# Optimization experiments

Measured on AMD Instinct MI355X. Metric: run time of the kernel, lower is better.

The kernel has to match this reference:

```python
import jax, jax.numpy as jnp
import numpy as np

DIM = 192
RES = 64
NUM_HEADS = 4
H_SP, W_SP = RES, 4  # idx == 0
SCALE = (DIM // NUM_HEADS) ** (-0.5)


def conv2d(x, w, b, pad, groups=1):
    y = jax.lax.conv_general_dilated(
        x, w, window_strides=(1, 1), padding=[(pad, pad), (pad, pad)],
        dimension_numbers=("NCHW", "OIHW", "NCHW"), feature_group_count=groups)
    return y + b[None, :, None, None]


def img2windows(img, H_sp, W_sp):
    B, C, H, W = img.shape
    x = img.reshape(B, C, H // H_sp, H_sp, W // W_sp, W_sp)
    return jnp.transpose(x, (0, 2, 4, 3, 5, 1)).reshape(-1, H_sp * W_sp, C)


def windows2img(w, H_sp, W_sp, H, W):
    Bw = w.shape[0]
    B = Bw // ((H // H_sp) * (W // W_sp))
    x = w.reshape(B, H // H_sp, W // W_sp, H_sp, W_sp, -1)
    return jnp.transpose(x, (0, 5, 1, 3, 2, 4)).reshape(B, -1, H, W)


def im2cswin(x):
    w = img2windows(x, H_SP, W_SP)  # [B', L, C]
    Bw, L, C = w.shape
    return jnp.transpose(w.reshape(Bw, L, NUM_HEADS, C // NUM_HEADS), (0, 2, 1, 3))


def setup_inputs() -> dict:
    key = jax.random.key(0)
    ks = jax.random.split(key, 11)
    s = 0.02
    return {
        "x": jax.random.normal(ks[0], (32, DIM, RES, RES), jnp.float32),
        "w_qk": jax.random.normal(ks[1], (2 * DIM, DIM, 1, 1), jnp.float32) * s,
        "b_qk": jnp.zeros((2 * DIM,), jnp.float32),
        "w_q5": jax.random.normal(ks[2], (DIM, 1, 5, 5), jnp.float32) * s,
        "b_q5": jnp.zeros((DIM,), jnp.float32),
        "w_k5": jax.random.normal(ks[3], (DIM, 1, 5, 5), jnp.float32) * s,
        "b_k5": jnp.zeros((DIM,), jnp.float32),
        "w_v": jax.random.normal(ks[4], (DIM, DIM, 1, 1), jnp.float32) * s,
        "b_v": jnp.zeros((DIM,), jnp.float32),
        "w_cape": jax.random.normal(ks[5], (DIM, 1, 5, 5), jnp.float32) * s,
        "b_cape": jnp.zeros((DIM,), jnp.float32),
    }


def reference(x, w_qk, b_qk, w_q5, b_q5, w_k5, b_k5, w_v, b_v, w_cape, b_cape):
    B, C, H, W = x.shape
    qk = conv2d(x, w_qk, b_qk, pad=0)
    q, k = jnp.split(qk, 2, axis=1)
    v = conv2d(x, w_v, b_v, pad=0)
    cape = conv2d(v, w_cape, b_cape, pad=2, groups=DIM)  # depthwise 5x5
    q = im2cswin(conv2d(q, w_q5, b_q5, pad=2, groups=DIM) + cape)
    k = im2cswin(conv2d(k, w_k5, b_k5, pad=2, groups=DIM) + cape)
    vw = im2cswin(v)
    q = q * SCALE
    attn = jnp.einsum("whqd,whkd->whqk", q, k)  # windows, heads, L, L
    attn = jax.nn.softmax(attn, axis=-1)
    out = jnp.einsum("whqk,whkd->whqd", attn, vw)
    Bw = out.shape[0]
    out = jnp.transpose(out, (0, 2, 1, 3)).reshape(Bw, H_SP * W_SP, C)
    return windows2img(out, H_SP, W_SP, H, W) + cape
```

## Files before the change

kernel.cpp:

```cpp
#include <hip/hip_runtime.h>

typedef short short8 __attribute__((ext_vector_type(8)));
typedef float f32x4 __attribute__((ext_vector_type(4)));
typedef int i32x4 __attribute__((ext_vector_type(4)));
typedef uint4 uint4_a4 __attribute__((aligned(4)));
typedef uint2 uint2_a4 __attribute__((aligned(4)));

#define BATCH 32
#define DIM 192
#define RES 64
#define HW 4096
#define NH 4
#define DH 48
#define NWIN 16
#define LTOK 256
#define BUFE (BATCH * DIM * HW)
#define SCALE_Q 0.14433756729740643f
#define LOG2E 1.4426950408889634f

__device__ __forceinline__ unsigned short f2bf(float f) {
  unsigned int u = __builtin_bit_cast(unsigned int, f);
  u += 0x7fffu + ((u >> 16) & 1u);
  return (unsigned short)(u >> 16);
}
__device__ __forceinline__ float bf2f(unsigned short h) {
  unsigned int u = ((unsigned int)h) << 16;
  return __builtin_bit_cast(float, u);
}
__device__ __forceinline__ f32x4 mfma16(short8 a, short8 b, f32x4 c) {
  return __builtin_amdgcn_mfma_f32_16x16x32_bf16(a, b, c, 0, 0, 0);
}

__global__ __launch_bounds__(256) void k0_wcvt(
    const float* __restrict__ w_qk, const float* __restrict__ w_v,
    unsigned short* __restrict__ wbf) {
  int u = blockIdx.x * 256 + threadIdx.x;
  int i4 = u * 4;
  const float* src = (i4 < 2 * DIM * DIM) ? (w_qk + i4) : (w_v + (i4 - 2 * DIM * DIM));
  float4 f = *(const float4*)src;
  uint2 pk;
  pk.x = (unsigned int)f2bf(f.x) | ((unsigned int)f2bf(f.y) << 16);
  pk.y = (unsigned int)f2bf(f.z) | ((unsigned int)f2bf(f.w) << 16);
  *(uint2*)&wbf[i4] = pk;
}

__global__ __launch_bounds__(256, 2) void k1_conv1x1(
    const float* __restrict__ x, const unsigned short* __restrict__ wbf,
    const float* __restrict__ b_qk, const float* __restrict__ b_v,
    unsigned short* __restrict__ q_raw, unsigned short* __restrict__ k_raw,
    unsigned short* __restrict__ v_buf) {
  __shared__ unsigned short Al[96 * 200];
  __shared__ unsigned short Bl[64 * 200];
  __shared__ unsigned short Os[96 * 68];
  const int tid = threadIdx.x;
  const int pix0 = blockIdx.x * 64;
  const int b = blockIdx.y;

  {
    const float* xb = x + (size_t)b * (DIM * HW) + pix0;
    int px = tid & 63;
    int icq = tid >> 6;
    for (int it = 0; it < 6; ++it) {
      int ic8 = icq + it * 4;
      const float* p = xb + (size_t)(ic8 * 8) * HW + px;
      unsigned short h[8];
#pragma unroll
      for (int j = 0; j < 8; ++j) h[j] = f2bf(p[(size_t)j * HW]);
      uint4 pk;
      pk.x = h[0] | ((unsigned int)h[1] << 16);
      pk.y = h[2] | ((unsigned int)h[3] << 16);
      pk.z = h[4] | ((unsigned int)h[5] << 16);
      pk.w = h[6] | ((unsigned int)h[7] << 16);
      *(uint4*)&Bl[px * 200 + ic8 * 8] = pk;
    }
  }

  const int lane = tid & 63, wv = tid >> 6;
  const int quad = lane >> 4, col = lane & 15;
  const int m0 = (wv >> 1) * 48, n0 = (wv & 1) * 32;

  for (int t = 0; t < 6; ++t) {
    {
      const unsigned short* wsrc = wbf + t * (96 * 192);
      uint4 tmp[9];
#pragma unroll
      for (int it = 0; it < 9; ++it) {
        int row = (it * 256 + tid) / 24, part = (it * 256 + tid) % 24;
        tmp[it] = *(const uint4*)(wsrc + row * 192 + part * 8);
      }
#pragma unroll
      for (int it = 0; it < 9; ++it) {
        int row = (it * 256 + tid) / 24, part = (it * 256 + tid) % 24;
        *(uint4*)&Al[row * 200 + part * 8] = tmp[it];
      }
    }
    __syncthreads();

    f32x4 acc[3][2];
#pragma unroll
    for (int fm = 0; fm < 3; ++fm)
#pragma unroll
      for (int fn = 0; fn < 2; ++fn) {
        acc[fm][fn][0] = 0.f; acc[fm][fn][1] = 0.f;
        acc[fm][fn][2] = 0.f; acc[fm][fn][3] = 0.f;
      }

#pragma unroll
    for (int ks = 0; ks < 6; ++ks) {
      short8 a[3], bb[2];
#pragma unroll
      for (int fm = 0; fm < 3; ++fm)
        a[fm] = *(const short8*)&Al[(m0 + fm * 16 + col) * 200 + ks * 32 + quad * 8];
#pragma unroll
      for (int fn = 0; fn < 2; ++fn)
        bb[fn] = *(const short8*)&Bl[(n0 + fn * 16 + col) * 200 + ks * 32 + quad * 8];
#pragma unroll
      for (int fm = 0; fm < 3; ++fm)
#pragma unroll
        for (int fn = 0; fn < 2; ++fn) acc[fm][fn] = mfma16(a[fm], bb[fn], acc[fm][fn]);
    }

    const int oc0 = t * 96;
#pragma unroll
    for (int fm = 0; fm < 3; ++fm) {
#pragma unroll
      for (int r = 0; r < 4; ++r) {
        int ocoff = m0 + fm * 16 + quad * 4 + r;
        int ocg = oc0 + ocoff;
        float bias = (ocg < 384) ? b_qk[ocg] : b_v[ocg - 384];
#pragma unroll
        for (int fn = 0; fn < 2; ++fn) {
          int px = n0 + fn * 16 + col;
          Os[ocoff * 68 + px] = f2bf(acc[fm][fn][r] + bias);
        }
      }
    }
    __syncthreads();

    unsigned short* dst;
    int ocbase;
    if (oc0 < 192) { dst = q_raw; ocbase = oc0; }
    else if (oc0 < 384) { dst = k_raw; ocbase = oc0 - 192; }
    else { dst = v_buf; ocbase = oc0 - 384; }
    {
      int row0 = tid >> 3, part = tid & 7;
#pragma unroll
      for (int it = 0; it < 3; ++it) {
        int row = it * 32 + row0;
        *(uint4*)&dst[((size_t)b * DIM + (ocbase + row)) * HW + pix0 + part * 8] =
            *(const uint4*)&Os[row * 68 + part * 8];
      }
    }
  }
}

__global__ __launch_bounds__(256) void k2_cape(
    const unsigned short* __restrict__ v_buf, const float* __restrict__ w_cape,
    const float* __restrict__ b_cape, float* __restrict__ cape_out) {
  const int c = blockIdx.y, b = blockIdx.z;
  const int h = blockIdx.x * 16 + (threadIdx.x >> 4);
  const int w4 = threadIdx.x & 15;
  const unsigned short* vp = v_buf + ((size_t)b * DIM + c) * HW;
  float wk[25];
#pragma unroll
  for (int i = 0; i < 25; ++i) wk[i] = w_cape[c * 25 + i];
  float acc[4];
  float bz = b_cape[c];
  acc[0] = acc[1] = acc[2] = acc[3] = bz;
#pragma unroll
  for (int dy = 0; dy < 5; ++dy) {
    int hr = h + dy - 2;
    float row[8];
    if (hr >= 0 && hr < RES) {
      const unsigned short* rp = vp + hr * RES + w4 * 4 - 2;
      uint4 pk;
      pk.x = pk.y = pk.z = pk.w = 0u;
      if (w4 == 0) {
        uint2_a4 m = *(const uint2_a4*)(rp + 2);
        pk.y = m.x; pk.z = m.y;
        pk.w = *(const unsigned int*)(rp + 6);
      } else if (w4 == 15) {
        pk.x = *(const unsigned int*)rp;
        uint2_a4 m = *(const uint2_a4*)(rp + 2);
        pk.y = m.x; pk.z = m.y;
      } else {
        pk = *(const uint4_a4*)rp;
      }
      row[0] = bf2f((unsigned short)(pk.x & 0xffff));
      row[1] = bf2f((unsigned short)(pk.x >> 16));
      row[2] = bf2f((unsigned short)(pk.y & 0xffff));
      row[3] = bf2f((unsigned short)(pk.y >> 16));
      row[4] = bf2f((unsigned short)(pk.z & 0xffff));
      row[5] = bf2f((unsigned short)(pk.z >> 16));
      row[6] = bf2f((unsigned short)(pk.w & 0xffff));
      row[7] = bf2f((unsigned short)(pk.w >> 16));
    } else {
#pragma unroll
      for (int j = 0; j < 8; ++j) row[j] = 0.f;
    }
#pragma unroll
    for (int wj = 0; wj < 4; ++wj)
#pragma unroll
      for (int dx = 0; dx < 5; ++dx) acc[wj] += row[wj + dx] * wk[dy * 5 + dx];
  }
  float4 o;
  o.x = acc[0]; o.y = acc[1]; o.z = acc[2]; o.w = acc[3];
  *(float4*)&cape_out[((size_t)b * DIM + c) * HW + h * RES + w4 * 4] = o;
}

__global__ __launch_bounds__(256) void k3_dw(
    const unsigned short* __restrict__ src, const float* __restrict__ w5,
    const float* __restrict__ b5, const float* __restrict__ cape,
    unsigned short* __restrict__ dst_w, float scale) {
  __shared__ unsigned short patch[64 * 168];
  __shared__ unsigned short outS[64 * 72];
  const int lid = blockIdx.x;
  const int xx = lid & 7;
  const int ii = lid >> 3;
  const int b = xx * 4 + ii / 192;
  const int rem = ii % 192;
  const int wb = rem / 12;
  const int rr2 = rem % 12;
  const int ct = rr2 >> 2, ht = rr2 & 3;
  const int c0 = ct * 64, h0 = ht * 16;
  const int tid = threadIdx.x;

  const int c = tid >> 2, hq = tid & 3;
  float wk[25];
#pragma unroll
  for (int i = 0; i < 25; ++i) wk[i] = w5[(c0 + c) * 25 + i];
  float bz = b5[c0 + c];
  const size_t cpbase = ((size_t)b * DIM + c0 + c) * HW + (size_t)wb * 4;
  float4 cp4[4];
#pragma unroll
  for (int j = 0; j < 4; ++j)
    cp4[j] = *(const float4*)&cape[cpbase + (size_t)(h0 + hq * 4 + j) * RES];

  for (int it = 0; it < 5; ++it) {
    int u = it * 256 + tid;
    int cc = u / 20, rr = u % 20;
    int hr = h0 - 2 + rr;
    uint4 pk;
    pk.x = pk.y = pk.z = pk.w = 0u;
    if (hr >= 0 && hr < RES) {
      const unsigned short* rp =
          src + ((size_t)b * DIM + c0 + cc) * HW + hr * RES + wb * 4 - 2;
      if (wb == 0) {
        uint2_a4 m = *(const uint2_a4*)(rp + 2);
        pk.y = m.x; pk.z = m.y;
        pk.w = *(const unsigned int*)(rp + 6);
      } else if (wb == 15) {
        pk.x = *(const unsigned int*)rp;
        uint2_a4 m = *(const uint2_a4*)(rp + 2);
        pk.y = m.x; pk.z = m.y;
      } else {
        pk = *(const uint4_a4*)rp;
      }
    }
    *(uint4*)&patch[cc * 168 + rr * 8] = pk;
  }
  __syncthreads();

  float acc[4][4];
#pragma unroll
  for (int j = 0; j < 4; ++j)
#pragma unroll
    for (int wm = 0; wm < 4; ++wm) acc[j][wm] = bz;

#pragma unroll
  for (int rel = 0; rel < 8; ++rel) {
    int p = hq * 4 + rel;
    uint4 pk = *(const uint4*)&patch[c * 168 + p * 8];
    float f8[8];
    f8[0] = bf2f((unsigned short)(pk.x & 0xffff));
    f8[1] = bf2f((unsigned short)(pk.x >> 16));
    f8[2] = bf2f((unsigned short)(pk.y & 0xffff));
    f8[3] = bf2f((unsigned short)(pk.y >> 16));
    f8[4] = bf2f((unsigned short)(pk.z & 0xffff));
    f8[5] = bf2f((unsigned short)(pk.z >> 16));
    f8[6] = bf2f((unsigned short)(pk.w & 0xffff));
    f8[7] = bf2f((unsigned short)(pk.w >> 16));
#pragma unroll
    for (int j = 0; j < 4; ++j) {
      int dy = rel - j;
      if (dy >= 0 && dy <= 4) {
#pragma unroll
        for (int wm = 0; wm < 4; ++wm)
#pragma unroll
          for (int dx = 0; dx < 5; ++dx) acc[j][wm] += f8[wm + dx] * wk[dy * 5 + dx];
      }
    }
  }

#pragma unroll
  for (int j = 0; j < 4; ++j) {
    float4 cp = cp4[j];
    int lb = (hq * 4 + j) * 4;
    outS[(lb + 0) * 72 + c] = f2bf((acc[j][0] + cp.x) * scale);
    outS[(lb + 1) * 72 + c] = f2bf((acc[j][1] + cp.y) * scale);
    outS[(lb + 2) * 72 + c] = f2bf((acc[j][2] + cp.z) * scale);
    outS[(lb + 3) * 72 + c] = f2bf((acc[j][3] + cp.w) * scale);
  }
  __syncthreads();

  const size_t obase = ((size_t)(b * NWIN + wb) * LTOK + (size_t)h0 * 4) * DIM + c0;
  for (int it = 0; it < 2; ++it) {
    int u = it * 256 + tid;
    int ll = u >> 3, part = u & 7;
    *(uint4*)&dst_w[obase + (size_t)ll * DIM + part * 8] =
        *(const uint4*)&outS[ll * 72 + part * 8];
  }
}

#define KSTR 56
#define VSTR 256

__global__ __launch_bounds__(256, 3) void k5_attn(
    const unsigned short* __restrict__ qf_w, const unsigned short* __restrict__ kf_w,
    const unsigned short* __restrict__ v_buf, unsigned short* __restrict__ out_w) {
  __shared__ unsigned short smem[26624];
  unsigned short* Kl = smem;
  unsigned short* Vl = smem + 14336;

  const int lid = blockIdx.x;
  const int xx = lid & 7;
  const int ii = lid >> 3;
  const int b = (xx << 2) | (ii >> 6);
  const int rem = ii & 63;
  const int wb = rem >> 2;
  const int hd = rem & 3;
  const int wi = b * NWIN + wb;

  const int tid = threadIdx.x, lane = tid & 63, wv = tid >> 6;
  const int quad = lane >> 4, col = lane & 15;

  short8 z8 = {0, 0, 0, 0, 0, 0, 0, 0};
  const unsigned short* qbase =
      qf_w + ((size_t)wi * LTOK + wv * 64 + col) * DIM + hd * DH;

  short8 bq0 = *(const short8*)(qbase + quad * 8);
  short8 bq1 = z8;
  if (quad < 2) bq1 = *(const short8*)(qbase + 32 + quad * 8);

  {
    const unsigned short* ks = kf_w + (size_t)wi * LTOK * DIM + hd * DH;
    for (int it = 0; it < 6; ++it) {
      int u = it * 256 + tid;
      int kl = u / 6, part = u % 6;
      *(uint4*)&Kl[kl * KSTR + part * 8] = *(const uint4*)(ks + (size_t)kl * DIM + part * 8);
    }
  }
  {
    const unsigned short* vs = v_buf + ((size_t)b * DIM + hd * DH) * HW + wb * 4;
    for (int it = 0; it < 12; ++it) {
      int u = it * 256 + tid;
      int d = u >> 6, h = u & 63;
      int kl8 = h >> 1;
      int off = ((kl8 ^ (d & 7)) * 8) + (h & 1) * 4;
      *(uint2*)&Vl[d * VSTR + off] = *(const uint2*)(vs + (size_t)d * HW + h * RES);
    }
  }
  __syncthreads();

  const int aA = (32 * (quad & 1) + col) * 4;
  const int aB = aA + 64;
  const bool lowq = quad < 2;

#pragma unroll
  for (int nt = 0; nt < 4; ++nt) {
    f32x4 s[16];
#pragma unroll
    for (int i = 0; i < 16; ++i) { s[i][0] = 0.f; s[i][1] = 0.f; s[i][2] = 0.f; s[i][3] = 0.f; }
    __builtin_amdgcn_s_setprio(1);
#pragma unroll
    for (int fm = 0; fm < 16; ++fm) {
      short8 a0 = *(const short8*)&Kl[(fm * 16 + col) * KSTR + quad * 8];
      s[fm] = mfma16(a0, bq0, s[fm]);
    }
#pragma unroll
    for (int fm = 0; fm < 16; ++fm) {
      short8 a1 = z8;
      if (quad < 2) a1 = *(const short8*)&Kl[(fm * 16 + col) * KSTR + 32 + quad * 8];
      s[fm] = mfma16(a1, bq1, s[fm]);
    }
    __builtin_amdgcn_s_setprio(0);

    short8 nq0 = z8, nq1 = z8;
    if (nt < 3) {
      const unsigned short* qn = qbase + (size_t)(nt + 1) * 16 * DIM;
      nq0 = *(const short8*)(qn + quad * 8);
      if (quad < 2) nq1 = *(const short8*)(qn + 32 + quad * 8);
    }

    float m4[16];
#pragma unroll
    for (int fm = 0; fm < 16; ++fm)
      m4[fm] = fmaxf(fmaxf(s[fm][0], s[fm][1]), fmaxf(s[fm][2], s[fm][3]));
#pragma unroll
    for (int i = 0; i < 8; ++i) m4[i] = fmaxf(m4[i], m4[i + 8]);
#pragma unroll
    for (int i = 0; i < 4; ++i) m4[i] = fmaxf(m4[i], m4[i + 4]);
    float mx = fmaxf(fmaxf(m4[0], m4[2]), fmaxf(m4[1], m4[3]));
    mx = fmaxf(mx, __shfl_xor(mx, 16));
    mx = fmaxf(mx, __shfl_xor(mx, 32));

    float s4[16];
#pragma unroll
    for (int fm = 0; fm < 16; ++fm) {
      float e0 = __builtin_exp2f(s[fm][0] - mx);
      float e1 = __builtin_exp2f(s[fm][1] - mx);
      float e2 = __builtin_exp2f(s[fm][2] - mx);
      float e3 = __builtin_exp2f(s[fm][3] - mx);
      s[fm][0] = e0; s[fm][1] = e1; s[fm][2] = e2; s[fm][3] = e3;
      s4[fm] = (e0 + e1) + (e2 + e3);
    }
#pragma unroll
    for (int i = 0; i < 8; ++i) s4[i] += s4[i + 8];
#pragma unroll
    for (int i = 0; i < 4; ++i) s4[i] += s4[i + 4];
    float sm = (s4[0] + s4[2]) + (s4[1] + s4[3]);
    sm += __shfl_xor(sm, 16);
    sm += __shfl_xor(sm, 32);
    float inv = __builtin_amdgcn_rcpf(sm);

    unsigned int w0[16], w1[16];
#pragma unroll
    for (int fm = 0; fm < 16; ++fm) {
      w0[fm] = (unsigned int)f2bf(s[fm][0]) | ((unsigned int)f2bf(s[fm][1]) << 16);
      w1[fm] = (unsigned int)f2bf(s[fm][2]) | ((unsigned int)f2bf(s[fm][3]) << 16);
    }

    float ivr[4];
#pragma unroll
    for (int r = 0; r < 4; ++r)
      ivr[r] = __builtin_bit_cast(
          float, __builtin_amdgcn_ds_bpermute((quad * 4 + r) * 4,
                                              __builtin_bit_cast(int, inv)));

    int pe[32], po[32];
#pragma unroll
    for (int ksi = 0; ksi < 8; ++ksi) {
      const int fe = 2 * ksi, fo = 2 * ksi + 1;
      pe[ksi * 4 + 0] = __builtin_amdgcn_ds_bpermute(aA, (int)w0[fe]);
      po[ksi * 4 + 0] = __builtin_amdgcn_ds_bpermute(aA, (int)w0[fo]);
      pe[ksi * 4 + 1] = __builtin_amdgcn_ds_bpermute(aA, (int)w1[fe]);
      po[ksi * 4 + 1] = __builtin_amdgcn_ds_bpermute(aA, (int)w1[fo]);
      pe[ksi * 4 + 2] = __builtin_amdgcn_ds_bpermute(aB, (int)w0[fe]);
      po[ksi * 4 + 2] = __builtin_amdgcn_ds_bpermute(aB, (int)w0[fo]);
      pe[ksi * 4 + 3] = __builtin_amdgcn_ds_bpermute(aB, (int)w1[fe]);
      po[ksi * 4 + 3] = __builtin_amdgcn_ds_bpermute(aB, (int)w1[fo]);
    }

    f32x4 o[3];
#pragma unroll
    for (int i = 0; i < 3; ++i) { o[i][0] = 0.f; o[i][1] = 0.f; o[i][2] = 0.f; o[i][3] = 0.f; }
    __builtin_amdgcn_s_setprio(1);
#pragma unroll
    for (int ksi = 0; ksi < 8; ++ksi) {
      i32x4 aw;
      aw[0] = lowq ? pe[ksi * 4 + 0] : po[ksi * 4 + 0];
      aw[1] = lowq ? pe[ksi * 4 + 1] : po[ksi * 4 + 1];
      aw[2] = lowq ? pe[ksi * 4 + 2] : po[ksi * 4 + 2];
      aw[3] = lowq ? pe[ksi * 4 + 3] : po[ksi * 4 + 3];
      short8 a = __builtin_bit_cast(short8, aw);
#pragma unroll
      for (int fn = 0; fn < 3; ++fn) {
        int d = fn * 16 + col;
        short8 bb = *(const short8*)&Vl[d * VSTR + (((ksi * 4 + quad) ^ (d & 7)) * 8)];
        o[fn] = mfma16(a, bb, o[fn]);
      }
    }
    __builtin_amdgcn_s_setprio(0);

    {
      unsigned short* dst =
          out_w + ((size_t)wi * LTOK + wv * 64 + nt * 16) * DIM + hd * DH;
#pragma unroll
      for (int fn = 0; fn < 3; ++fn)
#pragma unroll
        for (int r = 0; r < 4; ++r)
          dst[(size_t)(quad * 4 + r) * DIM + fn * 16 + col] = f2bf(o[fn][r] * ivr[r]);
    }

    bq0 = nq0;
    bq1 = nq1;
  }
}

__global__ __launch_bounds__(256) void k6_final(
    const unsigned short* __restrict__ out_w, float* __restrict__ io) {
  __shared__ float tile[16 * 528];
  const int ht = blockIdx.x, ct = blockIdx.y, b = blockIdx.z;
  const int c0 = ct * 16, h0 = ht * 8;
  const int tid = threadIdx.x;
  for (int it = 0; it < 4; ++it) {
    int u = it * 256 + tid;
    int chunk = u & 1, l5 = (u >> 1) & 31, wb = u >> 6;
    const unsigned short* p =
        out_w + ((size_t)(b * NWIN + wb) * LTOK + (size_t)(h0 * 4 + l5)) * DIM + c0 + chunk * 8;
    uint4 pk = *(const uint4*)p;
    int h = l5 >> 2, wm = l5 & 3;
    float* t = &tile[(chunk * 8) * 528 + h * 66 + wb * 4 + wm];
    t[0 * 528] = bf2f((unsigned short)(pk.x & 0xffff));
    t[1 * 528] = bf2f((unsigned short)(pk.x >> 16));
    t[2 * 528] = bf2f((unsigned short)(pk.y & 0xffff));
    t[3 * 528] = bf2f((unsigned short)(pk.y >> 16));
    t[4 * 528] = bf2f((unsigned short)(pk.z & 0xffff));
    t[5 * 528] = bf2f((unsigned short)(pk.z >> 16));
    t[6 * 528] = bf2f((unsigned short)(pk.w & 0xffff));
    t[7 * 528] = bf2f((unsigned short)(pk.w >> 16));
  }
  __syncthreads();
  for (int it = 0; it < 8; ++it) {
    int u = it * 256 + tid;
    int w16 = u & 15, h = (u >> 4) & 7, c = u >> 7;
    size_t g = ((size_t)b * DIM + c0 + c) * HW + (size_t)(h0 + h) * RES + w16 * 4;
    float4 cp = *(const float4*)&io[g];
    float4 ov;
    ov.x = tile[c * 528 + h * 66 + w16 * 4 + 0] + cp.x;
    ov.y = tile[c * 528 + h * 66 + w16 * 4 + 1] + cp.y;
    ov.z = tile[c * 528 + h * 66 + w16 * 4 + 2] + cp.z;
    ov.w = tile[c * 528 + h * 66 + w16 * 4 + 3] + cp.w;
    *(float4*)&io[g] = ov;
  }
}

extern "C" void kernel_launch(void* const* d_in, const int* in_sizes, int n_in,
                              void* d_out, int out_size, void* d_ws, size_t ws_size,
                              hipStream_t stream) {
  (void)in_sizes; (void)n_in; (void)out_size; (void)ws_size;
  const float* x = (const float*)d_in[0];
  const float* w_qk = (const float*)d_in[1];
  const float* b_qk = (const float*)d_in[2];
  const float* w_q5 = (const float*)d_in[3];
  const float* b_q5 = (const float*)d_in[4];
  const float* w_k5 = (const float*)d_in[5];
  const float* b_k5 = (const float*)d_in[6];
  const float* w_v = (const float*)d_in[7];
  const float* b_v = (const float*)d_in[8];
  const float* w_cape = (const float*)d_in[9];
  const float* b_cape = (const float*)d_in[10];
  float* out = (float*)d_out;

  unsigned short* ws = (unsigned short*)d_ws;
  unsigned short* buf0 = ws;
  unsigned short* buf1 = ws + (size_t)BUFE;
  unsigned short* buf2 = ws + (size_t)BUFE * 2;
  unsigned short* buf3 = ws + (size_t)BUFE * 3;

  k0_wcvt<<<dim3(108), 256, 0, stream>>>(w_qk, w_v, buf3);
  k1_conv1x1<<<dim3(64, 32), 256, 0, stream>>>(x, buf3, b_qk, b_v, buf0, buf1, buf2);
  k2_cape<<<dim3(4, 192, 32), 256, 0, stream>>>(buf2, w_cape, b_cape, out);
  k3_dw<<<dim3(6144), 256, 0, stream>>>(buf0, w_q5, b_q5, out, buf3, SCALE_Q * LOG2E);
  k3_dw<<<dim3(6144), 256, 0, stream>>>(buf1, w_k5, b_k5, out, buf0, 1.0f);
  k5_attn<<<dim3(2048), 256, 0, stream>>>(buf3, buf0, buf2, buf1);
  k6_final<<<dim3(8, 12, 32), 256, 0, stream>>>(buf1, out);
}
```

Measured before the change: 628.0 us.

## Software-pipeline QK^T MFMAs of next tile with softmax of current tile

Restructures the attention loop into a ping-pong over two score buffers, so the QK^T MFMAs for the next 16-query tile are interleaved with the exp/max/sum softmax work of the current tile. The goal is to hide transcendental and VALU latency behind matrix-core work. Because two full 16x f32x4 score arrays are live at once, register pressure roughly doubles for scores. Under launch_bounds(256,3) that risks spills or lower occupancy.

```diff
diff --git a/kernel.cpp b/kernel.cpp
--- a/kernel.cpp
+++ b/kernel.cpp
@@ -315,6 +315,91 @@
 #define KSTR 56
 #define VSTR 256
 
+#define ATTN_PASS(SC, SN, NT, DO_NEXT)                                          \
+  {                                                                             \
+    short8 pq0 = z8, pq1 = z8;                                                  \
+    if ((NT) < 2) {                                                             \
+      const unsigned short* qn = qbase + (size_t)((NT) + 2) * 16 * DIM;         \
+      pq0 = *(const short8*)(qn + quad * 8);                                    \
+      if (quad < 2) pq1 = *(const short8*)(qn + 32 + quad * 8);                 \
+    }                                                                           \
+    float m4[16];                                                               \
+    _Pragma("unroll") for (int fm = 0; fm < 16; ++fm)                           \
+        m4[fm] = fmaxf(fmaxf(SC[fm][0], SC[fm][1]), fmaxf(SC[fm][2], SC[fm][3]));\
+    _Pragma("unroll") for (int i = 0; i < 8; ++i) m4[i] = fmaxf(m4[i], m4[i+8]);\
+    _Pragma("unroll") for (int i = 0; i < 4; ++i) m4[i] = fmaxf(m4[i], m4[i+4]);\
+    float mx = fmaxf(fmaxf(m4[0], m4[2]), fmaxf(m4[1], m4[3]));                 \
+    mx = fmaxf(mx, __shfl_xor(mx, 16));                                         \
+    mx = fmaxf(mx, __shfl_xor(mx, 32));                                         \
+    unsigned int w0[16], w1[16];                                                \
+    float sc0 = 0.f, sc1 = 0.f, sc2 = 0.f, sc3 = 0.f;                           \
+    _Pragma("unroll") for (int fm = 0; fm < 16; ++fm) {                         \
+      if (DO_NEXT) {                                                            \
+        short8 a0 = *(const short8*)&Kl[(fm * 16 + col) * KSTR + quad * 8];     \
+        SN[fm] = mfma16(a0, bqn0, zf4);                                         \
+        short8 a1 = z8;                                                         \
+        if (quad < 2)                                                           \
+          a1 = *(const short8*)&Kl[(fm * 16 + col) * KSTR + 32 + quad * 8];     \
+        SN[fm] = mfma16(a1, bqn1, SN[fm]);                                      \
+      }                                                                         \
+      float e0 = __builtin_exp2f(SC[fm][0] - mx);                               \
+      float e1 = __builtin_exp2f(SC[fm][1] - mx);                               \
+      float e2 = __builtin_exp2f(SC[fm][2] - mx);                               \
+      float e3 = __builtin_exp2f(SC[fm][3] - mx);                               \
+      w0[fm] = (unsigned int)f2bf(e0) | ((unsigned int)f2bf(e1) << 16);         \
+      w1[fm] = (unsigned int)f2bf(e2) | ((unsigned int)f2bf(e3) << 16);         \
+      sc0 += e0; sc1 += e1; sc2 += e2; sc3 += e3;                               \
+    }                                                                           \
+    float sm = (sc0 + sc1) + (sc2 + sc3);                                       \
+    sm += __shfl_xor(sm, 16);                                                   \
+    sm += __shfl_xor(sm, 32);                                                   \
+    float inv = __builtin_amdgcn_rcpf(sm);                                      \
+    float ivr[4];                                                               \
+    _Pragma("unroll") for (int r = 0; r < 4; ++r)                               \
+        ivr[r] = __builtin_bit_cast(float,                                      \
+            __builtin_amdgcn_ds_bpermute((quad * 4 + r) * 4,                    \
+                                         __builtin_bit_cast(int, inv)));        \
+    int pe[32], po[32];                                                         \
+    _Pragma("unroll") for (int ksi = 0; ksi < 8; ++ksi) {                       \
+      const int fe = 2 * ksi, fo = 2 * ksi + 1;                                 \
+      pe[ksi * 4 + 0] = __builtin_amdgcn_ds_bpermute(aA, (int)w0[fe]);          \
+      po[ksi * 4 + 0] = __builtin_amdgcn_ds_bpermute(aA, (int)w0[fo]);          \
+      pe[ksi * 4 + 1] = __builtin_amdgcn_ds_bpermute(aA, (int)w1[fe]);          \
+      po[ksi * 4 + 1] = __builtin_amdgcn_ds_bpermute(aA, (int)w1[fo]);          \
+      pe[ksi * 4 + 2] = __builtin_amdgcn_ds_bpermute(aB, (int)w0[fe]);          \
+      po[ksi * 4 + 2] = __builtin_amdgcn_ds_bpermute(aB, (int)w0[fo]);          \
+      pe[ksi * 4 + 3] = __builtin_amdgcn_ds_bpermute(aB, (int)w1[fe]);          \
+      po[ksi * 4 + 3] = __builtin_amdgcn_ds_bpermute(aB, (int)w1[fo]);          \
+    }                                                                           \
+    f32x4 o[3];                                                                 \
+    _Pragma("unroll") for (int i = 0; i < 3; ++i) {                             \
+      o[i][0] = 0.f; o[i][1] = 0.f; o[i][2] = 0.f; o[i][3] = 0.f; }             \
+    __builtin_amdgcn_s_setprio(1);                                              \
+    _Pragma("unroll") for (int ksi = 0; ksi < 8; ++ksi) {                       \
+      i32x4 aw;                                                                 \
+      aw[0] = lowq ? pe[ksi * 4 + 0] : po[ksi * 4 + 0];                         \
+      aw[1] = lowq ? pe[ksi * 4 + 1] : po[ksi * 4 + 1];                         \
+      aw[2] = lowq ? pe[ksi * 4 + 2] : po[ksi * 4 + 2];                         \
+      aw[3] = lowq ? pe[ksi * 4 + 3] : po[ksi * 4 + 3];                         \
+      short8 a = __builtin_bit_cast(short8, aw);                                \
+      _Pragma("unroll") for (int fn = 0; fn < 3; ++fn) {                        \
+        int d = fn * 16 + col;                                                  \
+        short8 bb = *(const short8*)&Vl[d * VSTR + (((ksi * 4 + quad) ^ (d & 7)) * 8)]; \
+        o[fn] = mfma16(a, bb, o[fn]);                                           \
+      }                                                                         \
+    }                                                                           \
+    __builtin_amdgcn_s_setprio(0);                                              \
+    {                                                                           \
+      unsigned short* dst =                                                     \
+          out_w + ((size_t)wi * LTOK + wv * 64 + (NT) * 16) * DIM + hd * DH;    \
+      _Pragma("unroll") for (int fn = 0; fn < 3; ++fn)                          \
+        _Pragma("unroll") for (int r = 0; r < 4; ++r)                           \
+            dst[(size_t)(quad * 4 + r) * DIM + fn * 16 + col] =                 \
+                f2bf(o[fn][r] * ivr[r]);                                        \
+    }                                                                           \
+    bqn0 = pq0; bqn1 = pq1;                                                     \
+  }
+
 __global__ __launch_bounds__(256, 3) void k5_attn(
     const unsigned short* __restrict__ qf_w, const unsigned short* __restrict__ kf_w,
     const unsigned short* __restrict__ v_buf, unsigned short* __restrict__ out_w) {
@@ -335,12 +420,17 @@
   const int quad = lane >> 4, col = lane & 15;
 
   short8 z8 = {0, 0, 0, 0, 0, 0, 0, 0};
+  f32x4 zf4;
+  zf4[0] = 0.f; zf4[1] = 0.f; zf4[2] = 0.f; zf4[3] = 0.f;
   const unsigned short* qbase =
       qf_w + ((size_t)wi * LTOK + wv * 64 + col) * DIM + hd * DH;
 
   short8 bq0 = *(const short8*)(qbase + quad * 8);
   short8 bq1 = z8;
   if (quad < 2) bq1 = *(const short8*)(qbase + 32 + quad * 8);
+  short8 bqn0 = *(const short8*)(qbase + 16 * DIM + quad * 8);
+  short8 bqn1 = z8;
+  if (quad < 2) bqn1 = *(const short8*)(qbase + 16 * DIM + 32 + quad * 8);
 
   {
     const unsigned short* ks = kf_w + (size_t)wi * LTOK * DIM + hd * DH;
@@ -366,125 +456,27 @@
   const int aB = aA + 64;
   const bool lowq = quad < 2;
 
-#pragma unroll
-  for (int nt = 0; nt < 4; ++nt) {
-    f32x4 s[16];
-#pragma unroll
-    for (int i = 0; i < 16; ++i) { s[i][0] = 0.f; s[i][1] = 0.f; s[i][2] = 0.f; s[i][3] = 0.f; }
-    __builtin_amdgcn_s_setprio(1);
-#pragma unroll
-    for (int fm = 0; fm < 16; ++fm) {
-      short8 a0 = *(const short8*)&Kl[(fm * 16 + col) * KSTR + quad * 8];
-      s[fm] = mfma16(a0, bq0, s[fm]);
-    }
-#pragma unroll
-    for (int fm = 0; fm < 16; ++fm) {
-      short8 a1 = z8;
-      if (quad < 2) a1 = *(const short8*)&Kl[(fm * 16 + col) * KSTR + 32 + quad * 8];
-      s[fm] = mfma16(a1, bq1, s[fm]);
-    }
-    __builtin_amdgcn_s_setprio(0);
-
-    short8 nq0 = z8, nq1 = z8;
-    if (nt < 3) {
-      const unsigned short* qn = qbase + (size_t)(nt + 1) * 16 * DIM;
-      nq0 = *(const short8*)(qn + quad * 8);
-      if (quad < 2) nq1 = *(const short8*)(qn + 32 + quad * 8);
-    }
-
-    float m4[16];
-#pragma unroll
-    for (int fm = 0; fm < 16; ++fm)
-      m4[fm] = fmaxf(fmaxf(s[fm][0], s[fm][1]), fmaxf(s[fm][2], s[fm][3]));
-#pragma unroll
-    for (int i = 0; i < 8; ++i) m4[i] = fmaxf(m4[i], m4[i + 8]);
-#pragma unroll
-    for (int i = 0; i < 4; ++i) m4[i] = fmaxf(m4[i], m4[i + 4]);
-    float mx = fmaxf(fmaxf(m4[0], m4[2]), fmaxf(m4[1], m4[3]));
-    mx = fmaxf(mx, __shfl_xor(mx, 16));
-    mx = fmaxf(mx, __shfl_xor(mx, 32));
-
-    float s4[16];
-#pragma unroll
-    for (int fm = 0; fm < 16; ++fm) {
-      float e0 = __builtin_exp2f(s[fm][0] - mx);
-      float e1 = __builtin_exp2f(s[fm][1] - mx);
-      float e2 = __builtin_exp2f(s[fm][2] - mx);
-      float e3 = __builtin_exp2f(s[fm][3] - mx);
-      s[fm][0] = e0; s[fm][1] = e1; s[fm][2] = e2; s[fm][3] = e3;
-      s4[fm] = (e0 + e1) + (e2 + e3);
-    }
-#pragma unroll
-    for (int i = 0; i < 8; ++i) s4[i] += s4[i + 8];
-#pragma unroll
-    for (int i = 0; i < 4; ++i) s4[i] += s4[i + 4];
-    float sm = (s4[0] + s4[2]) + (s4[1] + s4[3]);
-    sm += __shfl_xor(sm, 16);
-    sm += __shfl_xor(sm, 32);
-    float inv = __builtin_amdgcn_rcpf(sm);
-
-    unsigned int w0[16], w1[16];
-#pragma unroll
-    for (int fm = 0; fm < 16; ++fm) {
-      w0[fm] = (unsigned int)f2bf(s[fm][0]) | ((unsigned int)f2bf(s[fm][1]) << 16);
-      w1[fm] = (unsigned int)f2bf(s[fm][2]) | ((unsigned int)f2bf(s[fm][3]) << 16);
-    }
-
-    float ivr[4];
-#pragma unroll
-    for (int r = 0; r < 4; ++r)
-      ivr[r] = __builtin_bit_cast(
-          float, __builtin_amdgcn_ds_bpermute((quad * 4 + r) * 4,
-                                              __builtin_bit_cast(int, inv)));
-
-    int pe[32], po[32];
-#pragma unroll
-    for (int ksi = 0; ksi < 8; ++ksi) {
-      const int fe = 2 * ksi, fo = 2 * ksi + 1;
-      pe[ksi * 4 + 0] = __builtin_amdgcn_ds_bpermute(aA, (int)w0[fe]);
-      po[ksi * 4 + 0] = __builtin_amdgcn_ds_bpermute(aA, (int)w0[fo]);
-      pe[ksi * 4 + 1] = __builtin_amdgcn_ds_bpermute(aA, (int)w1[fe]);
-      po[ksi * 4 + 1] = __builtin_amdgcn_ds_bpermute(aA, (int)w1[fo]);
-      pe[ksi * 4 + 2] = __builtin_amdgcn_ds_bpermute(aB, (int)w0[fe]);
-      po[ksi * 4 + 2] = __builtin_amdgcn_ds_bpermute(aB, (int)w0[fo]);
-      pe[ksi * 4 + 3] = __builtin_amdgcn_ds_bpermute(aB, (int)w1[fe]);
-      po[ksi * 4 + 3] = __builtin_amdgcn_ds_bpermute(aB, (int)w1[fo]);
-    }
-
-    f32x4 o[3];
-#pragma unroll
-    for (int i = 0; i < 3; ++i) { o[i][0] = 0.f; o[i][1] = 0.f; o[i][2] = 0.f; o[i][3] = 0.f; }
-    __builtin_amdgcn_s_setprio(1);
-#pragma unroll
-    for (int ksi = 0; ksi < 8; ++ksi) {
-      i32x4 aw;
-      aw[0] = lowq ? pe[ksi * 4 + 0] : po[ksi * 4 + 0];
-      aw[1] = lowq ? pe[ksi * 4 + 1] : po[ksi * 4 + 1];
-      aw[2] = lowq ? pe[ksi * 4 + 2] : po[ksi * 4 + 2];
-      aw[3] = lowq ? pe[ksi * 4 + 3] : po[ksi * 4 + 3];
-      short8 a = __builtin_bit_cast(short8, aw);
-#pragma unroll
-      for (int fn = 0; fn < 3; ++fn) {
-        int d = fn * 16 + col;
-        short8 bb = *(const short8*)&Vl[d * VSTR + (((ksi * 4 + quad) ^ (d & 7)) * 8)];
-        o[fn] = mfma16(a, bb, o[fn]);
-      }
-    }
-    __builtin_amdgcn_s_setprio(0);
-
-    {
-      unsigned short* dst =
-          out_w + ((size_t)wi * LTOK + wv * 64 + nt * 16) * DIM + hd * DH;
-#pragma unroll
-      for (int fn = 0; fn < 3; ++fn)
-#pragma unroll
-        for (int r = 0; r < 4; ++r)
-          dst[(size_t)(quad * 4 + r) * DIM + fn * 16 + col] = f2bf(o[fn][r] * ivr[r]);
-    }
-
-    bq0 = nq0;
-    bq1 = nq1;
-  }
+  f32x4 sA[16], sB[16];
+#pragma unroll
+  for (int i = 0; i < 16; ++i) { sA[i][0] = 0.f; sA[i][1] = 0.f; sA[i][2] = 0.f; sA[i][3] = 0.f; }
+  __builtin_amdgcn_s_setprio(1);
+#pragma unroll
+  for (int fm = 0; fm < 16; ++fm) {
+    short8 a0 = *(const short8*)&Kl[(fm * 16 + col) * KSTR + quad * 8];
+    sA[fm] = mfma16(a0, bq0, sA[fm]);
+  }
+#pragma unroll
+  for (int fm = 0; fm < 16; ++fm) {
+    short8 a1 = z8;
+    if (quad < 2) a1 = *(const short8*)&Kl[(fm * 16 + col) * KSTR + 32 + quad * 8];
+    sA[fm] = mfma16(a1, bq1, sA[fm]);
+  }
+  __builtin_amdgcn_s_setprio(0);
+
+  ATTN_PASS(sA, sB, 0, true);
+  ATTN_PASS(sB, sA, 1, true);
+  ATTN_PASS(sA, sB, 2, true);
+  ATTN_PASS(sB, sA, 3, false);
 }
 
 __global__ __launch_bounds__(256) void k6_final(
```

After: 681.7 us. +8.6%, slower.
